# Optimization experiments

Hardware: AMD Instinct MI355X
Metric: run time of the kernel (lower is better)

## Reference

```python
import jax, jax.numpy as jnp
import numpy as np

MODEL_DIM = 512
NUM_HEADS = 8
HEAD_DIM = 64
INNER = NUM_HEADS * HEAD_DIM  # 512 == MODEL_DIM -> projection is Identity


def setup_inputs() -> dict:
    key = jax.random.key(0)
    ks = jax.random.split(key, 7)
    B, T = 2, 4096
    x = jax.random.normal(ks[0], (B, T, MODEL_DIM), dtype=jnp.float32)
    s = 1.0 / np.sqrt(MODEL_DIM)
    Wq = jax.random.normal(ks[1], (MODEL_DIM, INNER), dtype=jnp.float32) * s
    Wk = jax.random.normal(ks[2], (MODEL_DIM, INNER), dtype=jnp.float32) * s
    Wv = jax.random.normal(ks[3], (MODEL_DIM, INNER), dtype=jnp.float32) * s
    bq = jax.random.normal(ks[4], (INNER,), dtype=jnp.float32) * 0.01
    bk = jax.random.normal(ks[5], (INNER,), dtype=jnp.float32) * 0.01
    bv = jax.random.normal(ks[6], (INNER,), dtype=jnp.float32) * 0.01
    return {"x": x, "Wq": Wq, "bq": bq, "Wk": Wk, "bk": bk, "Wv": Wv, "bv": bv}


def reference(x, Wq, bq, Wk, bk, Wv, bv):
    B, T, _ = x.shape
    # project and split heads: [B, H, T, D]
    q = (x @ Wq + bq).reshape(B, T, NUM_HEADS, HEAD_DIM).transpose(0, 2, 1, 3)
    k = (x @ Wk + bk).reshape(B, T, NUM_HEADS, HEAD_DIM).transpose(0, 2, 1, 3)
    v = (x @ Wv + bv).reshape(B, T, NUM_HEADS, HEAD_DIM).transpose(0, 2, 1, 3)
    scale = 1.0 / np.sqrt(HEAD_DIM).astype(np.float32)
    attn = jnp.einsum('bhqd,bhkd->bhqk', q, k) * scale  # [B,H,Tq,Tkv]
    attn = jax.nn.softmax(attn, axis=-1)
    out = jnp.einsum('bhqk,bhkd->bhqd', attn, v)        # [B,H,Tq,D]
    out = out.transpose(0, 2, 1, 3).reshape(B, T, INNER)
    return out  # projection is Identity since INNER == MODEL_DIM
```

## Files before the change

kernel.cpp:

```cpp
#include <hip/hip_runtime.h>
#include <hip/hip_bf16.h>


typedef __attribute__((ext_vector_type(8)))  _Float16 half8;
typedef __attribute__((ext_vector_type(2)))  __fp16   fp16x2;
typedef __attribute__((ext_vector_type(4)))  float    f32x4;
typedef __attribute__((ext_vector_type(16))) float    f32x16;
typedef __attribute__((ext_vector_type(2)))  int      i32x2;

#define TSEQ 4096
#define DH   64
#define NH   8
#define MD   512

#if __has_builtin(__builtin_amdgcn_exp2f)
__device__ inline float fexp2(float x){ return __builtin_amdgcn_exp2f(x); }
#else
__device__ inline float fexp2(float x){ float r; asm("v_exp_f32 %0, %1\n\ts_nop 1" : "=v"(r) : "v"(x)); return r; }
#endif

union H2U { fp16x2 h; unsigned int u; };
__device__ inline unsigned int pkrtz(float a, float b){
  H2U c; c.h = __builtin_amdgcn_cvt_pkrtz(a, b); return c.u;
}

#if __has_builtin(__builtin_amdgcn_permlane32_swap)
__device__ inline void plswap(unsigned int &a, unsigned int &b){
  i32x2 r = __builtin_amdgcn_permlane32_swap((int)a, (int)b, false, false);
  a = (unsigned int)r[0]; b = (unsigned int)r[1];
}
#else
__device__ inline void plswap(unsigned int &a, unsigned int &b){
  asm volatile("s_nop 1\n\tv_permlane32_swap_b32 %0, %1\n\ts_nop 1" : "+v"(a), "+v"(b));
}
#endif

union U4H8 { uint4 u; half8 h; };

#define AS3U(p) ((__attribute__((address_space(3))) unsigned int*)(p))
#define AS1U(p) ((const __attribute__((address_space(1))) unsigned int*)(p))

__global__ __launch_bounds__(256) void k_conv_x(const float* __restrict__ x, _Float16* __restrict__ xh){
  int i = (blockIdx.x*256 + threadIdx.x)*8;
  float4 a = *(const float4*)(x+i);
  float4 b = *(const float4*)(x+i+4);
  half8 o;
  o[0]=(_Float16)a.x; o[1]=(_Float16)a.y; o[2]=(_Float16)a.z; o[3]=(_Float16)a.w;
  o[4]=(_Float16)b.x; o[5]=(_Float16)b.y; o[6]=(_Float16)b.z; o[7]=(_Float16)b.w;
  *(half8*)(xh+i) = o;
}

__global__ __launch_bounds__(256) void k_prep_w(const float* __restrict__ Wq, const float* __restrict__ Wk,
                                                const float* __restrict__ Wv, _Float16* __restrict__ wt){
  __shared__ float tile[32][33];
  const int mat = blockIdx.z;
  const float* W = mat==0 ? Wq : (mat==1 ? Wk : Wv);
  const int n0 = blockIdx.x*32, k0 = blockIdx.y*32;
  const int tx = threadIdx.x & 31, ty = threadIdx.x >> 5;
  #pragma unroll
  for (int i=0;i<4;i++){ int k = ty*4+i; tile[k][tx] = W[(size_t)(k0+k)*MD + n0 + tx]; }
  __syncthreads();
  _Float16* dst = wt + (size_t)mat*MD*MD;
  #pragma unroll
  for (int i=0;i<4;i++){ int n = ty*4+i; dst[(size_t)(n0+n)*MD + k0 + tx] = (_Float16)tile[tx][n]; }
}

__global__ __launch_bounds__(256,2) void k_qkv(const _Float16* __restrict__ xh, const _Float16* __restrict__ wt,
              const float* __restrict__ bq, const float* __restrict__ bk, const float* __restrict__ bv,
              _Float16* __restrict__ qout, _Float16* __restrict__ kout, _Float16* __restrict__ vout){
  __shared__ alignas(16) _Float16 Ash[2][128*64];
  __shared__ alignas(16) _Float16 Bsh[2][128*64];
  const int tid = threadIdx.x, w = tid>>6, l = tid&63;
  const int fr = l&15, hi = l>>4;
  const int nt = blockIdx.x, mt = blockIdx.y;
  const int mat = nt>>2;
  const int n0  = (nt&3)*128;
  const int m0  = mt*128;
  const _Float16* W = wt + (size_t)mat*MD*MD;
  const int wr = (w>>1)*64, wc = (w&1)*64;

  f32x4 acc[4][4];
  #pragma unroll
  for (int a=0;a<4;a++)
    #pragma unroll
    for (int b=0;b<4;b++) acc[a][b] = (f32x4){0.f,0.f,0.f,0.f};

#define QSTAGE(k0_, buf) do { \
    _Pragma("unroll") \
    for (int i_=0;i_<4;i_++){ \
      int slot_ = tid + i_*256; \
      int row_ = slot_>>3, seg_ = (slot_&7) ^ (row_&7); \
      __builtin_amdgcn_global_load_lds(AS1U(xh + (size_t)(m0+row_)*MD + (k0_) + seg_*8), \
          AS3U((char*)&Ash[buf][0] + slot_*16), 16, 0, 0); \
      __builtin_amdgcn_global_load_lds(AS1U(W + (size_t)(n0+row_)*MD + (k0_) + seg_*8), \
          AS3U((char*)&Bsh[buf][0] + slot_*16), 16, 0, 0); \
    } \
  } while(0)

  QSTAGE(0, 0);

  for (int ks0=0; ks0<8; ks0++){
    const int cur = ks0&1;
    __syncthreads();
    if (ks0+1 < 8) QSTAGE((ks0+1)*64, cur^1);
    const _Float16* Ab = &Ash[cur][0];
    const _Float16* Bb = &Bsh[cur][0];
    #pragma unroll
    for (int ks=0;ks<2;ks++){
      half8 af[4], bfr[4];
      #pragma unroll
      for (int mi=0;mi<4;mi++){
        int row = wr + mi*16 + fr;
        af[mi] = *(const half8*)&Ab[row*64 + (((ks*4+hi) ^ (row&7))<<3)];
      }
      #pragma unroll
      for (int ni=0;ni<4;ni++){
        int row = wc + ni*16 + fr;
        bfr[ni] = *(const half8*)&Bb[row*64 + (((ks*4+hi) ^ (row&7))<<3)];
      }
      #pragma unroll
      for (int mi=0;mi<4;mi++)
        #pragma unroll
        for (int ni=0;ni<4;ni++)
          acc[mi][ni] = __builtin_amdgcn_mfma_f32_16x16x32_f16(af[mi], bfr[ni], acc[mi][ni], 0,0,0);
    }
  }
#undef QSTAGE

  const float* bias = mat==0 ? bq : (mat==1 ? bk : bv);
  const float scl = (mat==0) ? 0.125f*1.4426950408889634f : (mat==2 ? 0.0625f : 1.0f);
  if (mat==1){
    #pragma unroll
    for (int ni=0;ni<4;ni++){
      int n_in = n0 + wc + ni*16 + fr;
      float bb = bias[n_in];
      int h = n_in>>6, d = n_in&63;
      #pragma unroll
      for (int mi=0;mi<4;mi++)
        #pragma unroll
        for (int r=0;r<4;r++){
          int m = m0 + wr + mi*16 + hi*4 + r;
          float v = acc[mi][ni][r] + bb;
          int b_ = m>>12, t = m&4095;
          kout[ ((((size_t)(b_*NH + h))*8 + (d>>3))*TSEQ + t)*8 + (d&7) ] = (_Float16)v;
        }
    }
  } else {
    _Float16* dst = mat==0 ? qout : vout;
    #pragma unroll
    for (int ni=0;ni<4;ni++){
      int n_in = n0 + wc + ni*16 + fr;
      float bb = bias[n_in];
      int h = n_in>>6, d = n_in&63;
      #pragma unroll
      for (int mi=0;mi<4;mi++)
        #pragma unroll
        for (int r=0;r<4;r++){
          int m = m0 + wr + mi*16 + hi*4 + r;
          float v = (acc[mi][ni][r] + bb)*scl;
          int b_ = m>>12, t = m&4095;
          dst[ ((size_t)((b_*NH + h)*TSEQ + t))*DH + d ] = (_Float16)v;
        }
    }
  }
}

__global__ __launch_bounds__(256) void k_trans_v(const _Float16* __restrict__ v, _Float16* __restrict__ vtg){
  __shared__ _Float16 tile[64][72];
  const int tid = threadIdx.x;
  const int bh = blockIdx.y, t0 = blockIdx.x*64;
  const _Float16* src = v + ((size_t)bh*TSEQ + t0)*DH;
  #pragma unroll
  for (int i=0;i<2;i++){
    int slot = tid + i*256; int r = slot>>3, s = slot&7;
    *(half8*)&tile[r][s*8] = *(const half8*)(src + (size_t)r*DH + s*8);
  }
  __syncthreads();
  #pragma unroll
  for (int i=0;i<2;i++){
    int slot = tid + i*256;
    int d = slot&63, sg = slot>>6;
    half8 o;
    #pragma unroll
    for (int j=0;j<8;j++) o[j] = tile[sg*8+j][d];
    *(half8*)(vtg + (((size_t)bh*512 + (t0>>3) + sg)*64 + d)*8) = o;
  }
}

__global__ __launch_bounds__(256,2) void k_attn(const _Float16* __restrict__ qb_, const _Float16* __restrict__ ktg,
                                                const _Float16* __restrict__ vtg, float* __restrict__ out){
  __shared__ alignas(16) _Float16 Ksh[2*8192];
  __shared__ alignas(16) _Float16 Vsh[2*8192];
  const int tid = threadIdx.x, w = tid>>6, l = tid&63;
  const int ln31 = l&31, lh = l>>5;

  const int bid = blockIdx.x;
  const int swz = ((bid&7)<<6) | (bid>>3);
  const int bh = swz>>5, qblk = swz&31;

  const _Float16* Q  = qb_ + (size_t)bh*TSEQ*DH;
  const _Float16* Kt = ktg + (size_t)bh*8*TSEQ*8;
  const _Float16* Vt = vtg + (size_t)bh*512*64*8;
  const int q0 = qblk*128 + w*32;

  half8 qf[4];
  #pragma unroll
  for (int ds=0;ds<4;ds++)
    qf[ds] = *(const half8*)(Q + (size_t)(q0 + ln31)*DH + ds*16 + lh*8);

  f32x16 of0, of1;
  #pragma unroll
  for (int r=0;r<16;r++){ of0[r]=0.f; of1[r]=0.f; }
  float psum = 0.f;

  const int NT = TSEQ/128;
  const int kbase = lh*1024 + ln31*8;
  const int vbase = lh*512  + ln31*8;

#define STAGE(kt, buf) do { \
    const int k0_ = (kt)*128; \
    _Pragma("unroll") \
    for (int i_=0;i_<4;i_++){ \
      int base_ = i_*256 + w*64; \
      int slot_ = base_ + l; \
      int krow_ = slot_&127, kseg_ = slot_>>7; \
      __builtin_amdgcn_global_load_lds(AS1U(Kt + ((size_t)kseg_*TSEQ + k0_ + krow_)*8), \
          AS3U((char*)Ksh + (buf)*16384 + base_*16), 16, 0, 0); \
      __builtin_amdgcn_global_load_lds(AS1U(Vt + ((size_t)slot_ + k0_*8)*8), \
          AS3U((char*)Vsh + (buf)*16384 + base_*16), 16, 0, 0); \
    } \
  } while(0)

  STAGE(0, 0);

  for (int kt=0; kt<NT; kt++){
    const int cur = kt&1;
    __syncthreads();
    if (kt+1 < NT) STAGE(kt+1, cur^1);

    const _Float16* Kb = &Ksh[cur*8192];
    const _Float16* Vb = &Vsh[cur*8192];

    #pragma unroll
    for (int pair=0; pair<2; pair++){
      half8 kf[8], vf[8];
      #pragma unroll
      for (int ds=0;ds<4;ds++){
        kf[ds]   = *(const half8*)&Kb[kbase + ds*2048 + (pair*2+0)*256];
        kf[4+ds] = *(const half8*)&Kb[kbase + ds*2048 + (pair*2+1)*256];
      }
      #pragma unroll
      for (int ea=0;ea<4;ea++){
        vf[2*ea]   = *(const half8*)&Vb[vbase + (pair*4+ea)*1024];
        vf[2*ea+1] = *(const half8*)&Vb[vbase + (pair*4+ea)*1024 + 256];
      }

      f32x16 s0, s1;
      #pragma unroll
      for (int r=0;r<16;r++){ s0[r]=0.f; s1[r]=0.f; }
      #pragma unroll
      for (int ds=0;ds<4;ds++){
        s0 = __builtin_amdgcn_mfma_f32_32x32x16_f16(kf[ds],   qf[ds], s0, 0,0,0);
        s1 = __builtin_amdgcn_mfma_f32_32x32x16_f16(kf[4+ds], qf[ds], s1, 0,0,0);
      }

      unsigned int wv[16];
      #pragma unroll
      for (int m=0;m<2;m++){
        #pragma unroll
        for (int c=0;c<4;c++){
          float v0_ = m ? s1[4*c+0] : s0[4*c+0];
          float v1_ = m ? s1[4*c+1] : s0[4*c+1];
          float v2_ = m ? s1[4*c+2] : s0[4*c+2];
          float v3_ = m ? s1[4*c+3] : s0[4*c+3];
          float e0 = fexp2(v0_);
          float e1 = fexp2(v1_);
          float e2 = fexp2(v2_);
          float e3 = fexp2(v3_);
          psum += (e0+e1)+(e2+e3);
          wv[m*8+2*c+0] = pkrtz(e0, e1);
          wv[m*8+2*c+1] = pkrtz(e2, e3);
        }
      }

      #pragma unroll
      for (int m=0;m<2;m++){
        #pragma unroll
        for (int e=0;e<2;e++){
          unsigned int a0 = wv[m*8+4*e+0], a1 = wv[m*8+4*e+1];
          unsigned int b0 = wv[m*8+4*e+2], b1 = wv[m*8+4*e+3];
          plswap(a0, b0);
          plswap(a1, b1);
          U4H8 pf; pf.u.x=a0; pf.u.y=a1; pf.u.z=b0; pf.u.w=b1;
          const int sl = m*2 + e;
          of0 = __builtin_amdgcn_mfma_f32_32x32x16_f16(vf[2*sl],   pf.h, of0, 0,0,0);
          of1 = __builtin_amdgcn_mfma_f32_32x32x16_f16(vf[2*sl+1], pf.h, of1, 0,0,0);
        }
      }
    }
  }

  psum += __shfl_xor(psum, 32);
  float inv = 16.0f / psum;

  const int b_ = bh>>3, h = bh&7;
  float* o = out + ((size_t)(b_*TSEQ + q0 + ln31))*MD + h*DH;
  #pragma unroll
  for (int rr=0;rr<4;rr++){
    float4 o4 = { of0[4*rr+0]*inv, of0[4*rr+1]*inv, of0[4*rr+2]*inv, of0[4*rr+3]*inv };
    *(float4*)(o + rr*8 + lh*4) = o4;
  }
  #pragma unroll
  for (int rr=0;rr<4;rr++){
    float4 o4 = { of1[4*rr+0]*inv, of1[4*rr+1]*inv, of1[4*rr+2]*inv, of1[4*rr+3]*inv };
    *(float4*)(o + 32 + rr*8 + lh*4) = o4;
  }
#undef STAGE
}

extern "C" void kernel_launch(void* const* d_in, const int* in_sizes, int n_in,
                              void* d_out, int out_size, void* d_ws, size_t ws_size,
                              hipStream_t stream) {
  const float* x  = (const float*)d_in[0];
  const float* Wq = (const float*)d_in[1];
  const float* bq = (const float*)d_in[2];
  const float* Wk = (const float*)d_in[3];
  const float* bk = (const float*)d_in[4];
  const float* Wv = (const float*)d_in[5];
  const float* bv = (const float*)d_in[6];
  float* out = (float*)d_out;

  char* ws = (char*)d_ws;
  _Float16* xh = (_Float16*)(ws);
  _Float16* wt = (_Float16*)(ws + ((size_t)8<<20));
  _Float16* qb = (_Float16*)(ws + ((size_t)10<<20));
  _Float16* kb = (_Float16*)(ws + ((size_t)18<<20));
  _Float16* vb = (_Float16*)(ws + ((size_t)26<<20));
  _Float16* vt = xh;

  k_conv_x<<<2048, 256, 0, stream>>>(x, xh);
  k_prep_w<<<dim3(16,16,3), 256, 0, stream>>>(Wq, Wk, Wv, wt);
  k_qkv<<<dim3(12,64), 256, 0, stream>>>(xh, wt, bq, bk, bv, qb, kb, vb);
  k_trans_v<<<dim3(64,16), 256, 0, stream>>>(vb, vt);
  k_attn<<<512, 256, 0, stream>>>(qb, kb, vt, out);
}
```

Baseline: 125.8 us.

## Fuse prep kernels and write transposed V directly from QKV epilogue

The x conversion and weight transpose kernels are merged into one launch, using block-index ranges to pick the task. The separate V transpose kernel is removed: the QKV GEMM epilogue now writes V straight into the blocked transposed layout that attention consumes. The first score MFMA now takes a zero constant as its accumulator instead of a per-iteration zero-initialised vector. This saves two launches and a full round trip of V through memory, at the cost of scattered 2-byte stores in the V epilogue.

```diff
diff --git a/kernel.cpp b/kernel.cpp
--- a/kernel.cpp
+++ b/kernel.cpp
@@ -40,22 +40,26 @@
 #define AS3U(p) ((__attribute__((address_space(3))) unsigned int*)(p))
 #define AS1U(p) ((const __attribute__((address_space(1))) unsigned int*)(p))
 
-__global__ __launch_bounds__(256) void k_conv_x(const float* __restrict__ x, _Float16* __restrict__ xh){
-  int i = (blockIdx.x*256 + threadIdx.x)*8;
-  float4 a = *(const float4*)(x+i);
-  float4 b = *(const float4*)(x+i+4);
-  half8 o;
-  o[0]=(_Float16)a.x; o[1]=(_Float16)a.y; o[2]=(_Float16)a.z; o[3]=(_Float16)a.w;
-  o[4]=(_Float16)b.x; o[5]=(_Float16)b.y; o[6]=(_Float16)b.z; o[7]=(_Float16)b.w;
-  *(half8*)(xh+i) = o;
-}
-
-__global__ __launch_bounds__(256) void k_prep_w(const float* __restrict__ Wq, const float* __restrict__ Wk,
-                                                const float* __restrict__ Wv, _Float16* __restrict__ wt){
+__global__ __launch_bounds__(256) void k_prep(const float* __restrict__ x, _Float16* __restrict__ xh,
+                                              const float* __restrict__ Wq, const float* __restrict__ Wk,
+                                              const float* __restrict__ Wv, _Float16* __restrict__ wt){
+  const int bid = blockIdx.x;
+  if (bid < 2048){
+    int i = (bid*256 + threadIdx.x)*8;
+    float4 a = *(const float4*)(x+i);
+    float4 b = *(const float4*)(x+i+4);
+    half8 o;
+    o[0]=(_Float16)a.x; o[1]=(_Float16)a.y; o[2]=(_Float16)a.z; o[3]=(_Float16)a.w;
+    o[4]=(_Float16)b.x; o[5]=(_Float16)b.y; o[6]=(_Float16)b.z; o[7]=(_Float16)b.w;
+    *(half8*)(xh+i) = o;
+    return;
+  }
   __shared__ float tile[32][33];
-  const int mat = blockIdx.z;
+  const int bid2 = bid - 2048;
+  const int mat = bid2 >> 8;
+  const int rem = bid2 & 255;
   const float* W = mat==0 ? Wq : (mat==1 ? Wk : Wv);
-  const int n0 = blockIdx.x*32, k0 = blockIdx.y*32;
+  const int n0 = (rem&15)*32, k0 = (rem>>4)*32;
   const int tx = threadIdx.x & 31, ty = threadIdx.x >> 5;
   #pragma unroll
   for (int i=0;i<4;i++){ int k = ty*4+i; tile[k][tx] = W[(size_t)(k0+k)*MD + n0 + tx]; }
@@ -128,7 +132,6 @@
 #undef QSTAGE
 
   const float* bias = mat==0 ? bq : (mat==1 ? bk : bv);
-  const float scl = (mat==0) ? 0.125f*1.4426950408889634f : (mat==2 ? 0.0625f : 1.0f);
   if (mat==1){
     #pragma unroll
     for (int ni=0;ni<4;ni++){
@@ -145,8 +148,7 @@
           kout[ ((((size_t)(b_*NH + h))*8 + (d>>3))*TSEQ + t)*8 + (d&7) ] = (_Float16)v;
         }
     }
-  } else {
-    _Float16* dst = mat==0 ? qout : vout;
+  } else if (mat==2){
     #pragma unroll
     for (int ni=0;ni<4;ni++){
       int n_in = n0 + wc + ni*16 + fr;
@@ -157,33 +159,28 @@
         #pragma unroll
         for (int r=0;r<4;r++){
           int m = m0 + wr + mi*16 + hi*4 + r;
+          float v = (acc[mi][ni][r] + bb)*0.0625f;
+          int b_ = m>>12, t = m&4095;
+          vout[ ((((size_t)(b_*NH + h))*512 + (t>>3))*64 + d)*8 + (t&7) ] = (_Float16)v;
+        }
+    }
+  } else {
+    const float scl = 0.125f*1.4426950408889634f;
+    #pragma unroll
+    for (int ni=0;ni<4;ni++){
+      int n_in = n0 + wc + ni*16 + fr;
+      float bb = bias[n_in];
+      int h = n_in>>6, d = n_in&63;
+      #pragma unroll
+      for (int mi=0;mi<4;mi++)
+        #pragma unroll
+        for (int r=0;r<4;r++){
+          int m = m0 + wr + mi*16 + hi*4 + r;
           float v = (acc[mi][ni][r] + bb)*scl;
           int b_ = m>>12, t = m&4095;
-          dst[ ((size_t)((b_*NH + h)*TSEQ + t))*DH + d ] = (_Float16)v;
-        }
-    }
-  }
-}
-
-__global__ __launch_bounds__(256) void k_trans_v(const _Float16* __restrict__ v, _Float16* __restrict__ vtg){
-  __shared__ _Float16 tile[64][72];
-  const int tid = threadIdx.x;
-  const int bh = blockIdx.y, t0 = blockIdx.x*64;
-  const _Float16* src = v + ((size_t)bh*TSEQ + t0)*DH;
-  #pragma unroll
-  for (int i=0;i<2;i++){
-    int slot = tid + i*256; int r = slot>>3, s = slot&7;
-    *(half8*)&tile[r][s*8] = *(const half8*)(src + (size_t)r*DH + s*8);
-  }
-  __syncthreads();
-  #pragma unroll
-  for (int i=0;i<2;i++){
-    int slot = tid + i*256;
-    int d = slot&63, sg = slot>>6;
-    half8 o;
-    #pragma unroll
-    for (int j=0;j<8;j++) o[j] = tile[sg*8+j][d];
-    *(half8*)(vtg + (((size_t)bh*512 + (t0>>3) + sg)*64 + d)*8) = o;
+          qout[ ((size_t)((b_*NH + h)*TSEQ + t))*DH + d ] = (_Float16)v;
+        }
+    }
   }
 }
 
@@ -211,6 +208,7 @@
   f32x16 of0, of1;
   #pragma unroll
   for (int r=0;r<16;r++){ of0[r]=0.f; of1[r]=0.f; }
+  const f32x16 fzero = of0;
   float psum = 0.f;
 
   const int NT = TSEQ/128;
@@ -255,11 +253,10 @@
         vf[2*ea+1] = *(const half8*)&Vb[vbase + (pair*4+ea)*1024 + 256];
       }
 
-      f32x16 s0, s1;
-      #pragma unroll
-      for (int r=0;r<16;r++){ s0[r]=0.f; s1[r]=0.f; }
-      #pragma unroll
-      for (int ds=0;ds<4;ds++){
+      f32x16 s0 = __builtin_amdgcn_mfma_f32_32x32x16_f16(kf[0], qf[0], fzero, 0,0,0);
+      f32x16 s1 = __builtin_amdgcn_mfma_f32_32x32x16_f16(kf[4], qf[0], fzero, 0,0,0);
+      #pragma unroll
+      for (int ds=1;ds<4;ds++){
         s0 = __builtin_amdgcn_mfma_f32_32x32x16_f16(kf[ds],   qf[ds], s0, 0,0,0);
         s1 = __builtin_amdgcn_mfma_f32_32x32x16_f16(kf[4+ds], qf[ds], s1, 0,0,0);
       }
@@ -335,12 +332,9 @@
   _Float16* wt = (_Float16*)(ws + ((size_t)8<<20));
   _Float16* qb = (_Float16*)(ws + ((size_t)10<<20));
   _Float16* kb = (_Float16*)(ws + ((size_t)18<<20));
-  _Float16* vb = (_Float16*)(ws + ((size_t)26<<20));
-  _Float16* vt = xh;
-
-  k_conv_x<<<2048, 256, 0, stream>>>(x, xh);
-  k_prep_w<<<dim3(16,16,3), 256, 0, stream>>>(Wq, Wk, Wv, wt);
-  k_qkv<<<dim3(12,64), 256, 0, stream>>>(xh, wt, bq, bk, bv, qb, kb, vb);
-  k_trans_v<<<dim3(64,16), 256, 0, stream>>>(vb, vt);
-  k_attn<<<512, 256, 0, stream>>>(qb, kb, vt, out);
-}
+  _Float16* vtg= (_Float16*)(ws + ((size_t)26<<20));
+
+  k_prep<<<2816, 256, 0, stream>>>(x, xh, Wq, Wk, Wv, wt);
+  k_qkv<<<dim3(12,64), 256, 0, stream>>>(xh, wt, bq, bk, bv, qb, kb, vtg);
+  k_attn<<<512, 256, 0, stream>>>(qb, kb, vtg, out);
+}
```

After: 114.6 us. 1.1x faster.
